# Optimization experiments

Hardware: AMD Instinct MI355X
Metric: run time of the kernel (lower is better)

Reference implementation:

```python
import jax, jax.numpy as jnp
import numpy as np

N_NODES = 50000
N_EDGES = 800000
IN_FEAT = 128
HID = 128
OUT = 10
N_GRAPHS = 128
BN_EPS = 1e-5


def setup_inputs() -> dict:
    key = jax.random.key(0)
    ks = jax.random.split(key, 16)
    inp = {
        "n_feat": jax.random.normal(ks[0], (N_NODES, IN_FEAT), dtype=jnp.float32),
        "src": jax.random.randint(ks[1], (N_EDGES,), 0, N_NODES),
        "dst": jax.random.randint(ks[2], (N_EDGES,), 0, N_NODES),
        "graph_ids": jnp.sort(jax.random.randint(ks[3], (N_NODES,), 0, N_GRAPHS)),
        # GraphConv weights (DGL layout: weight [in, out], bias [out])
        "W1": jax.random.normal(ks[4], (IN_FEAT, HID), dtype=jnp.float32) / np.sqrt(IN_FEAT),
        "b1": jnp.zeros((HID,), dtype=jnp.float32),
        "W2": jax.random.normal(ks[5], (HID, HID), dtype=jnp.float32) / np.sqrt(HID),
        "b2": jnp.zeros((HID,), dtype=jnp.float32),
        # BatchNorm1d affine params
        "gamma": jnp.ones((HID,), dtype=jnp.float32),
        "beta": jnp.zeros((HID,), dtype=jnp.float32),
        # MLP head
        "fc1_w": jax.random.normal(ks[6], (HID, HID), dtype=jnp.float32) / np.sqrt(HID),
        "fc1_b": jnp.zeros((HID,), dtype=jnp.float32),
        "fc2_w": jax.random.normal(ks[7], (HID, OUT), dtype=jnp.float32) / np.sqrt(HID),
        "fc2_b": jnp.zeros((OUT,), dtype=jnp.float32),
    }
    return inp


def _graph_conv(x, W, b, src, dst, inv_sqrt_out, inv_sqrt_in):
    # DGL GraphConv, norm='both': h = D_in^{-1/2} A D_out^{-1/2} x W + b
    h = x * inv_sqrt_out[:, None]          # [N, d_in]
    h = h @ W                              # [N, d_out] (project before gather: fewer bytes moved)
    agg = jax.ops.segment_sum(h[src], dst, num_segments=N_NODES)  # gather + scatter-add
    return agg * inv_sqrt_in[:, None] + b


def reference(n_feat, src, dst, graph_ids, W1, b1, W2, b2, gamma, beta,
              fc1_w, fc1_b, fc2_w, fc2_b):
    ones_e = jnp.ones((N_EDGES,), dtype=jnp.float32)
    deg_out = jnp.clip(jax.ops.segment_sum(ones_e, src, num_segments=N_NODES), 1.0)
    deg_in = jnp.clip(jax.ops.segment_sum(ones_e, dst, num_segments=N_NODES), 1.0)
    inv_sqrt_out = jax.lax.rsqrt(deg_out)
    inv_sqrt_in = jax.lax.rsqrt(deg_in)

    x = jax.nn.relu(_graph_conv(n_feat, W1, b1, src, dst, inv_sqrt_out, inv_sqrt_in))
    # dropout is identity in eval mode
    x = jax.nn.relu(_graph_conv(x, W2, b2, src, dst, inv_sqrt_out, inv_sqrt_in))

    # SumPooling over graphs
    embedding = jax.ops.segment_sum(x, graph_ids, num_segments=N_GRAPHS)  # [B, HID]

    # BatchNorm1d (training-mode batch stats, biased variance like torch)
    mu = jnp.mean(embedding, axis=0)
    var = jnp.mean(jnp.square(embedding - mu), axis=0)
    h = gamma * (embedding - mu) * jax.lax.rsqrt(var + BN_EPS) + beta

    h = jax.nn.relu(h @ fc1_w + fc1_b)
    logits = h @ fc2_w + fc2_b
    return embedding, jax.nn.log_softmax(logits, axis=-1)
```

## Files before the change

kernel.cpp:

```cpp
#include <hip/hip_runtime.h>
#include <hip/hip_bf16.h>
#include <math.h>

#define N_NODES 50000
#define N_EDGES 800000
#define HID 128
#define N_GRAPHS 128
#define OUTC 10
#define BN_EPS 1e-5f

#define SCAN_B 256
#define N_SCAN_BLOCKS ((N_NODES + SCAN_B - 1) / SCAN_B)

#define POOL_CHUNK 32
#define N_POOL_BLOCKS ((N_NODES + POOL_CHUNK - 1) / POOL_CHUNK)

#define HB 80
#define HWORDS (N_NODES / 2)
#define HR_B 128
#define HR_BLOCKS ((HWORDS + HR_B - 1) / HR_B)

#define EPAD 8
#define E_SRC_CAP (N_EDGES + N_NODES * EPAD)

#define LDA 136

#define MM1_ROWS 320
#define MM1_SLICES (MM1_ROWS / 16)
#define MM1_TILES ((N_NODES + 1 + MM1_ROWS - 1) / MM1_ROWS)

#define AGG_NODES 16
#define AGG_BLOCKS (N_NODES / AGG_NODES)

typedef short short8 __attribute__((ext_vector_type(8)));
typedef float floatx4 __attribute__((ext_vector_type(4)));

template <typename T, typename F>
__device__ inline T bitcast(F f) {
    union { F a; T b; } u;
    u.a = f;
    return u.b;
}

__device__ inline unsigned short f2bf(float x) {
    return __hip_bfloat16_raw(__float2bfloat16(x)).x;
}

__global__ __launch_bounds__(1024) void hist_part_kernel(const int* __restrict__ src,
                                                         const int* __restrict__ dst,
                                                         unsigned int* __restrict__ part,
                                                         const float* __restrict__ W1,
                                                         const float* __restrict__ W2,
                                                         unsigned short* __restrict__ Wp) {
    if (blockIdx.x == 2 * HB) {
        for (int q = threadIdx.x; q < 4096; q += 1024) {
            int wi = q >> 11;
            const float* __restrict__ W = wi ? W2 : W1;
            int t2 = q & 2047;
            int tile = t2 >> 6, lane = t2 & 63;
            int kc = tile >> 3, nt = tile & 7;
            int n = lane & 15, quad = lane >> 4;
            unsigned short v[8];
#pragma unroll
            for (int j = 0; j < 8; j++) {
                int k = kc * 32 + quad * 8 + j;
                v[j] = f2bf(W[k * HID + nt * 16 + n]);
            }
            *(uint4*)&Wp[(size_t)q * 8] = *(uint4*)v;
        }
        return;
    }
    __shared__ unsigned int h[HWORDS];
    for (int i = threadIdx.x; i < HWORDS; i += 1024) h[i] = 0;
    __syncthreads();
    int half = (blockIdx.x >= HB) ? 1 : 0;
    const int* __restrict__ idx = half ? dst : src;
    int b = blockIdx.x - half * HB;
    for (int e = b * 1024 + threadIdx.x; e < N_EDGES; e += HB * 1024) {
        int v = idx[e];
        atomicAdd(&h[v >> 1], 1u << ((v & 1) << 4));
    }
    __syncthreads();
    unsigned int* __restrict__ out = part + (size_t)blockIdx.x * HWORDS;
    for (int i = threadIdx.x; i < HWORDS; i += 1024) out[i] = h[i];
}

__global__ __launch_bounds__(HR_B) void hist_reduce_kernel(unsigned int* __restrict__ part,
                                                           int* __restrict__ cnt_in,
                                                           float* __restrict__ inv_out,
                                                           float* __restrict__ inv_in,
                                                           int* __restrict__ bsum) {
    int w = blockIdx.x * HR_B + threadIdx.x;
    int padsum = 0;
    if (w < HWORDS) {
        unsigned int s = 0, d = 0;
        for (int b = 0; b < HB; b++) {
            s += part[(size_t)b * HWORDS + w];
            unsigned int c = part[(size_t)(b + HB) * HWORDS + w];
            part[(size_t)(b + HB) * HWORDS + w] = d;
            d += c;
        }
        int i0 = w * 2, i1 = i0 + 1;
        int so0 = (int)(s & 0xFFFFu), so1 = (int)(s >> 16);
        int di0 = (int)(d & 0xFFFFu), di1 = (int)(d >> 16);
        cnt_in[i0] = di0;
        cnt_in[i1] = di1;
        inv_out[i0] = rsqrtf(fmaxf((float)so0, 1.0f));
        inv_out[i1] = rsqrtf(fmaxf((float)so1, 1.0f));
        inv_in[i0] = rsqrtf(fmaxf((float)di0, 1.0f));
        inv_in[i1] = rsqrtf(fmaxf((float)di1, 1.0f));
        padsum = ((di0 + EPAD - 1) & ~(EPAD - 1)) + ((di1 + EPAD - 1) & ~(EPAD - 1));
    }
    __shared__ int red[HR_B];
    red[threadIdx.x] = padsum;
    __syncthreads();
    for (int o = HR_B / 2; o > 0; o >>= 1) {
        if (threadIdx.x < o) red[threadIdx.x] += red[threadIdx.x + o];
        __syncthreads();
    }
    if (threadIdx.x == 0) bsum[blockIdx.x] = red[0];
}

__global__ void scan_write_kernel(const int* __restrict__ cnt, const int* __restrict__ bsum,
                                  int* __restrict__ row_ptr, int* __restrict__ edge_src) {
    __shared__ int sb[SCAN_B];
    __shared__ int part[SCAN_B];
    int t = threadIdx.x;
    sb[t] = (t < N_SCAN_BLOCKS) ? bsum[t] : 0;
    __syncthreads();
    for (int off = 1; off < SCAN_B; off <<= 1) {
        int u = (t >= off) ? sb[t - off] : 0;
        __syncthreads();
        sb[t] += u;
        __syncthreads();
    }
    int boff = (blockIdx.x == 0) ? 0 : sb[blockIdx.x - 1];

    int i = blockIdx.x * SCAN_B + t;
    int raw = (i < N_NODES) ? cnt[i] : 0;
    int v = (raw + EPAD - 1) & ~(EPAD - 1);
    part[t] = v;
    __syncthreads();
    for (int off = 1; off < SCAN_B; off <<= 1) {
        int u = (t >= off) ? part[t - off] : 0;
        __syncthreads();
        part[t] += u;
        __syncthreads();
    }
    if (i < N_NODES) {
        int ex = part[t] - v + boff;
        row_ptr[i] = ex;
        for (int p = ex + raw; p < ex + v; p++) edge_src[p] = N_NODES;
        if (i == N_NODES - 1) row_ptr[N_NODES] = ex + v;
    }
}

__device__ inline void mm_slice16(const unsigned short* __restrict__ xs,
                                  const unsigned short* __restrict__ Wp,
                                  __hip_bfloat16* __restrict__ Y, int row0, int rowl) {
    int lane = threadIdx.x & 63;
    int m = lane & 15, quad = lane >> 4;

    short8 a[4];
#pragma unroll
    for (int kc = 0; kc < 4; kc++)
        a[kc] = bitcast<short8>(*(const uint4*)&xs[(rowl + m) * LDA + kc * 32 + quad * 8]);

    floatx4 acc[8];
#pragma unroll
    for (int nt = 0; nt < 8; nt++) acc[nt] = (floatx4){0.f, 0.f, 0.f, 0.f};

#pragma unroll
    for (int nt = 0; nt < 8; nt++) {
#pragma unroll
        for (int kc = 0; kc < 4; kc++) {
            short8 bfr = bitcast<short8>(
                *(const uint4*)&Wp[((size_t)(kc * 8 + nt) * 64 + lane) * 8]);
            acc[nt] = __builtin_amdgcn_mfma_f32_16x16x32_bf16(a[kc], bfr, acc[nt], 0, 0, 0);
        }
    }

#pragma unroll
    for (int nt = 0; nt < 8; nt++) {
#pragma unroll
        for (int i = 0; i < 4; i++) {
            int rg = row0 + rowl + quad * 4 + i;
            if (rg < N_NODES + 1) {
                Y[(size_t)rg * HID + nt * 16 + m] = __float2bfloat16(acc[nt][i]);
            }
        }
    }
}

__global__ __launch_bounds__(1024) void csrmm1_kernel(const int* __restrict__ src,
                                                      const int* __restrict__ dst,
                                                      const unsigned int* __restrict__ part,
                                                      const int* __restrict__ row_ptr,
                                                      int* __restrict__ edge_src,
                                                      const float* __restrict__ X,
                                                      const float* __restrict__ scale,
                                                      const unsigned short* __restrict__ Wp,
                                                      __hip_bfloat16* __restrict__ Y,
                                                      float* __restrict__ emb) {
    __shared__ unsigned int shb[HWORDS];
    int t = threadIdx.x, b = blockIdx.x;

    if (b < HB) {
        unsigned int* loc = shb;
        const unsigned int* __restrict__ off = part + (size_t)(b + HB) * HWORDS;
        for (int i = t; i < HWORDS; i += 1024) loc[i] = off[i];
        __syncthreads();
        for (int e = b * 1024 + t; e < N_EDGES; e += HB * 1024) {
            int d = dst[e];
            unsigned int old = atomicAdd(&loc[d >> 1], 1u << ((d & 1) << 4));
            int local = (d & 1) ? (int)(old >> 16) : (int)(old & 0xFFFFu);
            edge_src[row_ptr[d] + local] = src[e];
        }
        return;
    }
    if (b == HB + MM1_TILES) {
        for (int i = t; i < N_GRAPHS * HID; i += 1024) emb[i] = 0.f;
        return;
    }

    unsigned short* xs = (unsigned short*)shb;
    int row0 = (b - HB) * MM1_ROWS;
    for (int j = 0; j < MM1_ROWS / 32; j++) {
        int idx4 = j * 1024 + t;
        int r = idx4 >> 5;
        int col = (idx4 & 31) * 4;
        int rg = row0 + r;
        float4 v = make_float4(0.f, 0.f, 0.f, 0.f);
        if (rg < N_NODES) {
            v = *(const float4*)&X[(size_t)rg * HID + col];
            float sc = scale[rg];
            v.x *= sc; v.y *= sc; v.z *= sc; v.w *= sc;
        }
        unsigned short o[4];
        o[0] = f2bf(v.x); o[1] = f2bf(v.y); o[2] = f2bf(v.z); o[3] = f2bf(v.w);
        *(ushort4*)&xs[r * LDA + col] = *(ushort4*)o;
    }
    __syncthreads();
    int wave = t >> 6;
    for (int sl = wave; sl < MM1_SLICES; sl += 16)
        mm_slice16(xs, Wp, Y, row0, sl * 16);
}

#define ACC8(u)                                                                              \
    acc[0] += __uint_as_float(u.x << 16); acc[1] += __uint_as_float(u.x & 0xFFFF0000u);      \
    acc[2] += __uint_as_float(u.y << 16); acc[3] += __uint_as_float(u.y & 0xFFFF0000u);      \
    acc[4] += __uint_as_float(u.z << 16); acc[5] += __uint_as_float(u.z & 0xFFFF0000u);      \
    acc[6] += __uint_as_float(u.w << 16); acc[7] += __uint_as_float(u.w & 0xFFFF0000u);

__global__ __launch_bounds__(256) void agg1mm2_kernel(const __hip_bfloat16* __restrict__ Y1,
                                                      const int* __restrict__ edge_src,
                                                      const int* __restrict__ row_ptr,
                                                      const float* __restrict__ inv_in,
                                                      const float* __restrict__ inv_out,
                                                      const float* __restrict__ bias,
                                                      const unsigned short* __restrict__ Wp2,
                                                      __hip_bfloat16* __restrict__ Y2) {
    if (blockIdx.x == AGG_BLOCKS) {
        if (threadIdx.x < 16) {
            uint4 z = make_uint4(0u, 0u, 0u, 0u);
            *(uint4*)&Y2[(size_t)N_NODES * HID + threadIdx.x * 8] = z;
        }
        return;
    }
    __shared__ unsigned short xs[AGG_NODES * LDA];
    const uint4* __restrict__ Yq = (const uint4*)Y1;
    int wave = threadIdx.x >> 6;
    int lane = threadIdx.x & 63;
    int esub = lane >> 4;
    int f16 = lane & 15;

    for (int it = 0; it < 4; it++) {
        int n = blockIdx.x * AGG_NODES + wave * 4 + it;
        int beg = row_ptr[n], end = row_ptr[n + 1];
        float acc[8] = {};
        for (int base = beg; base < end; base += 64) {
            int mm = min(64, end - base);
            int idx = (lane < mm) ? edge_src[base + lane] : N_NODES;
            int j = 0;
            for (; j + 16 <= mm; j += 16) {
                int s0 = __shfl(idx, j + esub);
                int s1 = __shfl(idx, j + 4 + esub);
                int s2 = __shfl(idx, j + 8 + esub);
                int s3 = __shfl(idx, j + 12 + esub);
                uint4 u0 = Yq[s0 * (HID / 8) + f16];
                uint4 u1 = Yq[s1 * (HID / 8) + f16];
                uint4 u2 = Yq[s2 * (HID / 8) + f16];
                uint4 u3 = Yq[s3 * (HID / 8) + f16];
                ACC8(u0); ACC8(u1); ACC8(u2); ACC8(u3);
            }
            if (j < mm) {
                int s0 = __shfl(idx, j + esub);
                int s1 = __shfl(idx, j + 4 + esub);
                uint4 u0 = Yq[s0 * (HID / 8) + f16];
                uint4 u1 = Yq[s1 * (HID / 8) + f16];
                ACC8(u0); ACC8(u1);
            }
        }
#pragma unroll
        for (int i = 0; i < 8; i++) {
            acc[i] += __shfl_xor(acc[i], 16);
            acc[i] += __shfl_xor(acc[i], 32);
        }
        if (lane < 16) {
            float si = inv_in[n];
            float so = inv_out[n];
            int f0 = f16 * 8;
            float4 b0 = *(const float4*)&bias[f0];
            float4 b1 = *(const float4*)&bias[f0 + 4];
            unsigned short u[8];
            u[0] = f2bf(fmaxf(acc[0] * si + b0.x, 0.f) * so);
            u[1] = f2bf(fmaxf(acc[1] * si + b0.y, 0.f) * so);
            u[2] = f2bf(fmaxf(acc[2] * si + b0.z, 0.f) * so);
            u[3] = f2bf(fmaxf(acc[3] * si + b0.w, 0.f) * so);
            u[4] = f2bf(fmaxf(acc[4] * si + b1.x, 0.f) * so);
            u[5] = f2bf(fmaxf(acc[5] * si + b1.y, 0.f) * so);
            u[6] = f2bf(fmaxf(acc[6] * si + b1.z, 0.f) * so);
            u[7] = f2bf(fmaxf(acc[7] * si + b1.w, 0.f) * so);
            *(uint4*)&xs[(wave * 4 + it) * LDA + f0] = *(uint4*)u;
        }
    }
    __syncthreads();

    int m = lane & 15, quad = lane >> 4;
    short8 a[4];
#pragma unroll
    for (int kc = 0; kc < 4; kc++)
        a[kc] = bitcast<short8>(*(const uint4*)&xs[m * LDA + kc * 32 + quad * 8]);
#pragma unroll
    for (int w2 = 0; w2 < 2; w2++) {
        int nt = wave * 2 + w2;
        floatx4 acc2 = (floatx4){0.f, 0.f, 0.f, 0.f};
#pragma unroll
        for (int kc = 0; kc < 4; kc++) {
            short8 bfr = bitcast<short8>(
                *(const uint4*)&Wp2[((size_t)(kc * 8 + nt) * 64 + lane) * 8]);
            acc2 = __builtin_amdgcn_mfma_f32_16x16x32_bf16(a[kc], bfr, acc2, 0, 0, 0);
        }
#pragma unroll
        for (int i = 0; i < 4; i++) {
            int rg = blockIdx.x * AGG_NODES + quad * 4 + i;
            Y2[(size_t)rg * HID + nt * 16 + m] = __float2bfloat16(acc2[i]);
        }
    }
}

__global__ __launch_bounds__(256) void agg2_kernel(const __hip_bfloat16* __restrict__ Y,
                                                   const int* __restrict__ edge_src,
                                                   const int* __restrict__ row_ptr,
                                                   const float* __restrict__ inv_in,
                                                   const float* __restrict__ bias,
                                                   float* __restrict__ Xout) {
    const uint4* __restrict__ Yq = (const uint4*)Y;
    int wave = threadIdx.x >> 6;
    int lane = threadIdx.x & 63;
    int n = blockIdx.x * 4 + wave;
    if (n >= N_NODES) return;
    int beg = row_ptr[n], end = row_ptr[n + 1];
    int esub = lane >> 4;
    int f16 = lane & 15;
    float acc[8] = {};
    for (int base = beg; base < end; base += 64) {
        int mm = min(64, end - base);
        int idx = (lane < mm) ? edge_src[base + lane] : N_NODES;
        int j = 0;
        for (; j + 16 <= mm; j += 16) {
            int s0 = __shfl(idx, j + esub);
            int s1 = __shfl(idx, j + 4 + esub);
            int s2 = __shfl(idx, j + 8 + esub);
            int s3 = __shfl(idx, j + 12 + esub);
            uint4 u0 = Yq[s0 * (HID / 8) + f16];
            uint4 u1 = Yq[s1 * (HID / 8) + f16];
            uint4 u2 = Yq[s2 * (HID / 8) + f16];
            uint4 u3 = Yq[s3 * (HID / 8) + f16];
            ACC8(u0); ACC8(u1); ACC8(u2); ACC8(u3);
        }
        if (j < mm) {
            int s0 = __shfl(idx, j + esub);
            int s1 = __shfl(idx, j + 4 + esub);
            uint4 u0 = Yq[s0 * (HID / 8) + f16];
            uint4 u1 = Yq[s1 * (HID / 8) + f16];
            ACC8(u0); ACC8(u1);
        }
    }
#pragma unroll
    for (int i = 0; i < 8; i++) {
        acc[i] += __shfl_xor(acc[i], 16);
        acc[i] += __shfl_xor(acc[i], 32);
    }
    if (lane < 16) {
        float si = inv_in[n];
        int f0 = f16 * 8;
        float4 b0 = *(const float4*)&bias[f0];
        float4 b1 = *(const float4*)&bias[f0 + 4];
        float4 o0, o1;
        o0.x = fmaxf(acc[0] * si + b0.x, 0.f);
        o0.y = fmaxf(acc[1] * si + b0.y, 0.f);
        o0.z = fmaxf(acc[2] * si + b0.z, 0.f);
        o0.w = fmaxf(acc[3] * si + b0.w, 0.f);
        o1.x = fmaxf(acc[4] * si + b1.x, 0.f);
        o1.y = fmaxf(acc[5] * si + b1.y, 0.f);
        o1.z = fmaxf(acc[6] * si + b1.z, 0.f);
        o1.w = fmaxf(acc[7] * si + b1.w, 0.f);
        *(float4*)&Xout[(size_t)n * HID + f0] = o0;
        *(float4*)&Xout[(size_t)n * HID + f0 + 4] = o1;
    }
}

__global__ __launch_bounds__(64) void pool_kernel(const float* __restrict__ X,
                                                  const int* __restrict__ gid,
                                                  float* __restrict__ emb) {
    int lane = threadIdx.x;
    int n0 = blockIdx.x * POOL_CHUNK;
    int n1 = min(n0 + POOL_CHUNK, N_NODES);
    if (n0 >= N_NODES) return;
    int g_cur = gid[n0];
    float ax = 0.f, ay = 0.f;
    for (int n = n0; n < n1; n++) {
        int g = gid[n];
        if (g != g_cur) {
            atomicAdd(&emb[g_cur * HID + lane * 2], ax);
            atomicAdd(&emb[g_cur * HID + lane * 2 + 1], ay);
            ax = 0.f; ay = 0.f;
            g_cur = g;
        }
        float2 v = *(const float2*)&X[(size_t)n * HID + lane * 2];
        ax += v.x;
        ay += v.y;
    }
    atomicAdd(&emb[g_cur * HID + lane * 2], ax);
    atomicAdd(&emb[g_cur * HID + lane * 2 + 1], ay);
}

__global__ __launch_bounds__(128) void head_fused_kernel(const float* __restrict__ emb,
                                                         const float* __restrict__ gamma,
                                                         const float* __restrict__ beta,
                                                         const float* __restrict__ fc1_w,
                                                         const float* __restrict__ fc1_b,
                                                         const float* __restrict__ fc2_w,
                                                         const float* __restrict__ fc2_b,
                                                         float* __restrict__ out) {
    int r = blockIdx.x, f = threadIdx.x;
    float s = 0.f;
    for (int row = 0; row < N_GRAPHS; row++) s += emb[row * HID + f];
    float mu = s * (1.f / N_GRAPHS);
    float v = 0.f;
    for (int row = 0; row < N_GRAPHS; row++) {
        float d = emb[row * HID + f] - mu;
        v += d * d;
    }
    v *= (1.f / N_GRAPHS);
    float sc = gamma[f] * rsqrtf(v + BN_EPS);
    float sh = beta[f] - mu * sc;

    __shared__ float xr[HID];
    xr[f] = emb[r * HID + f] * sc + sh;
    __syncthreads();
    float acc = fc1_b[f];
    for (int k = 0; k < HID; k++) acc += xr[k] * fc1_w[k * HID + f];
    __shared__ float hr[HID];
    hr[f] = fmaxf(acc, 0.f);
    __syncthreads();

    __shared__ float logits[OUTC];
    __shared__ float mstat[2];
    if (f < OUTC) {
        float a = fc2_b[f];
        for (int k = 0; k < HID; k++) a += hr[k] * fc2_w[k * OUTC + f];
        logits[f] = a;
    }
    __syncthreads();
    if (f == 0) {
        float m = logits[0];
        for (int o = 1; o < OUTC; o++) m = fmaxf(m, logits[o]);
        float sum = 0.f;
        for (int o = 0; o < OUTC; o++) sum += expf(logits[o] - m);
        mstat[0] = m;
        mstat[1] = logf(sum);
    }
    __syncthreads();
    if (f < OUTC) out[r * OUTC + f] = logits[f] - mstat[0] - mstat[1];
}

extern "C" void kernel_launch(void* const* d_in, const int* in_sizes, int n_in,
                              void* d_out, int out_size, void* d_ws, size_t ws_size,
                              hipStream_t stream) {
    const float* n_feat = (const float*)d_in[0];
    const int*   src    = (const int*)d_in[1];
    const int*   dst    = (const int*)d_in[2];
    const int*   gid    = (const int*)d_in[3];
    const float* W1     = (const float*)d_in[4];
    const float* b1     = (const float*)d_in[5];
    const float* W2     = (const float*)d_in[6];
    const float* b2     = (const float*)d_in[7];
    const float* gamma  = (const float*)d_in[8];
    const float* beta   = (const float*)d_in[9];
    const float* fc1_w  = (const float*)d_in[10];
    const float* fc1_b  = (const float*)d_in[11];
    const float* fc2_w  = (const float*)d_in[12];
    const float* fc2_b  = (const float*)d_in[13];

    char* wsb = (char*)d_ws;
    size_t off = 0;
    auto alloc = [&](size_t bytes) -> void* {
        void* p = wsb + off;
        off += (bytes + 255) & ~(size_t)255;
        return p;
    };
    int*   cnt_in  = (int*)alloc((size_t)N_NODES * 4);
    int*   row_ptr = (int*)alloc((size_t)(N_NODES + 1) * 4);
    int*   e_src   = (int*)alloc((size_t)E_SRC_CAP * 4);
    float* inv_out = (float*)alloc((size_t)N_NODES * 4);
    float* inv_in  = (float*)alloc((size_t)N_NODES * 4);
    unsigned int* part = (unsigned int*)alloc((size_t)2 * HB * HWORDS * 4);
    __hip_bfloat16* Y1 = (__hip_bfloat16*)alloc((size_t)(N_NODES + 1) * HID * 2);
    __hip_bfloat16* Y2 = (__hip_bfloat16*)alloc((size_t)(N_NODES + 1) * HID * 2);
    float* X       = (float*)alloc((size_t)N_NODES * HID * 4);
    unsigned short* Wp = (unsigned short*)alloc((size_t)2 * 32 * 64 * 8 * 2);
    int*   bsum    = (int*)alloc((size_t)SCAN_B * 4);

    float* emb_out = (float*)d_out;
    float* lsm_out = emb_out + N_GRAPHS * HID;

    hist_part_kernel<<<2 * HB + 1, 1024, 0, stream>>>(src, dst, part, W1, W2, Wp);
    hist_reduce_kernel<<<HR_BLOCKS, HR_B, 0, stream>>>(part, cnt_in, inv_out, inv_in, bsum);
    scan_write_kernel<<<N_SCAN_BLOCKS, SCAN_B, 0, stream>>>(cnt_in, bsum, row_ptr, e_src);
    csrmm1_kernel<<<HB + MM1_TILES + 1, 1024, 0, stream>>>(src, dst, part, row_ptr, e_src,
                                                           n_feat, inv_out, Wp, Y1, emb_out);
    agg1mm2_kernel<<<AGG_BLOCKS + 1, 256, 0, stream>>>(Y1, e_src, row_ptr, inv_in, inv_out,
                                                       b1, Wp + (size_t)32 * 64 * 8, Y2);
    agg2_kernel<<<(N_NODES + 3) / 4, 256, 0, stream>>>(Y2, e_src, row_ptr, inv_in, b2, X);

    pool_kernel<<<N_POOL_BLOCKS, 64, 0, stream>>>(X, gid, emb_out);
    head_fused_kernel<<<N_GRAPHS, HID, 0, stream>>>(emb_out, gamma, beta, fc1_w, fc1_b,
                                                    fc2_w, fc2_b, lsm_out);
}
```

Baseline: 257.7 us.

## Fuse degree scan with first projection GEMM and split CSR fill into own kernel

The prefix scan that builds row_ptr now runs in the same launch as the first feature projection (X*inv_out @ W1), which only depends on inv_out. The projection uses 64-row tiles with 256-thread blocks instead of 320-row tiles with 1024 threads. The CSR edge fill, which needs row_ptr, moves into its own kernel after this launch. This regrouping keeps the kernel count the same while hiding the serial scan behind GEMM work and giving the GEMM smaller blocks that need less shared memory, so occupancy can rise. The fill kernel still needs its large shared histogram and no longer overlaps with the GEMM.

```diff
diff --git a/kernel.cpp b/kernel.cpp
--- a/kernel.cpp
+++ b/kernel.cpp
@@ -25,9 +25,7 @@
 
 #define LDA 136
 
-#define MM1_ROWS 320
-#define MM1_SLICES (MM1_ROWS / 16)
-#define MM1_TILES ((N_NODES + 1 + MM1_ROWS - 1) / MM1_ROWS)
+#define MM_BLOCKS ((N_NODES + 64) / 64)
 
 #define AGG_NODES 16
 #define AGG_BLOCKS (N_NODES / AGG_NODES)
@@ -121,45 +119,13 @@
     if (threadIdx.x == 0) bsum[blockIdx.x] = red[0];
 }
 
-__global__ void scan_write_kernel(const int* __restrict__ cnt, const int* __restrict__ bsum,
-                                  int* __restrict__ row_ptr, int* __restrict__ edge_src) {
-    __shared__ int sb[SCAN_B];
-    __shared__ int part[SCAN_B];
-    int t = threadIdx.x;
-    sb[t] = (t < N_SCAN_BLOCKS) ? bsum[t] : 0;
-    __syncthreads();
-    for (int off = 1; off < SCAN_B; off <<= 1) {
-        int u = (t >= off) ? sb[t - off] : 0;
-        __syncthreads();
-        sb[t] += u;
-        __syncthreads();
-    }
-    int boff = (blockIdx.x == 0) ? 0 : sb[blockIdx.x - 1];
-
-    int i = blockIdx.x * SCAN_B + t;
-    int raw = (i < N_NODES) ? cnt[i] : 0;
-    int v = (raw + EPAD - 1) & ~(EPAD - 1);
-    part[t] = v;
-    __syncthreads();
-    for (int off = 1; off < SCAN_B; off <<= 1) {
-        int u = (t >= off) ? part[t - off] : 0;
-        __syncthreads();
-        part[t] += u;
-        __syncthreads();
-    }
-    if (i < N_NODES) {
-        int ex = part[t] - v + boff;
-        row_ptr[i] = ex;
-        for (int p = ex + raw; p < ex + v; p++) edge_src[p] = N_NODES;
-        if (i == N_NODES - 1) row_ptr[N_NODES] = ex + v;
-    }
-}
-
-__device__ inline void mm_slice16(const unsigned short* __restrict__ xs,
-                                  const unsigned short* __restrict__ Wp,
-                                  __hip_bfloat16* __restrict__ Y, int row0, int rowl) {
-    int lane = threadIdx.x & 63;
+__device__ inline void mm_tail(const unsigned short* __restrict__ xs,
+                               const unsigned short* __restrict__ Wp,
+                               __hip_bfloat16* __restrict__ Y, int row0) {
+    int tid = threadIdx.x;
+    int wave = tid >> 6, lane = tid & 63;
     int m = lane & 15, quad = lane >> 4;
+    int rowl = wave * 16;
 
     short8 a[4];
 #pragma unroll
@@ -192,58 +158,92 @@
     }
 }
 
-__global__ __launch_bounds__(1024) void csrmm1_kernel(const int* __restrict__ src,
-                                                      const int* __restrict__ dst,
-                                                      const unsigned int* __restrict__ part,
-                                                      const int* __restrict__ row_ptr,
+__global__ __launch_bounds__(256) void scanmm1_kernel(const int* __restrict__ cnt,
+                                                      const int* __restrict__ bsum,
+                                                      int* __restrict__ row_ptr,
                                                       int* __restrict__ edge_src,
                                                       const float* __restrict__ X,
                                                       const float* __restrict__ scale,
                                                       const unsigned short* __restrict__ Wp,
                                                       __hip_bfloat16* __restrict__ Y,
                                                       float* __restrict__ emb) {
-    __shared__ unsigned int shb[HWORDS];
-    int t = threadIdx.x, b = blockIdx.x;
-
-    if (b < HB) {
-        unsigned int* loc = shb;
-        const unsigned int* __restrict__ off = part + (size_t)(b + HB) * HWORDS;
-        for (int i = t; i < HWORDS; i += 1024) loc[i] = off[i];
+    __shared__ unsigned short xs[64 * LDA];
+    int t = threadIdx.x;
+    int b = blockIdx.x;
+
+    if (b >= N_SCAN_BLOCKS) {
+        if (b == N_SCAN_BLOCKS + MM_BLOCKS) {
+            for (int i = t; i < N_GRAPHS * HID; i += 256) emb[i] = 0.f;
+            return;
+        }
+        int row0 = (b - N_SCAN_BLOCKS) * 64;
+        for (int j = 0; j < 8; j++) {
+            int idx4 = j * 256 + t;
+            int r = idx4 >> 5;
+            int col = (idx4 & 31) * 4;
+            int rg = row0 + r;
+            float4 v = make_float4(0.f, 0.f, 0.f, 0.f);
+            if (rg < N_NODES) {
+                v = *(const float4*)&X[(size_t)rg * HID + col];
+                float sc = scale[rg];
+                v.x *= sc; v.y *= sc; v.z *= sc; v.w *= sc;
+            }
+            unsigned short o[4];
+            o[0] = f2bf(v.x); o[1] = f2bf(v.y); o[2] = f2bf(v.z); o[3] = f2bf(v.w);
+            *(ushort4*)&xs[r * LDA + col] = *(ushort4*)o;
+        }
         __syncthreads();
-        for (int e = b * 1024 + t; e < N_EDGES; e += HB * 1024) {
-            int d = dst[e];
-            unsigned int old = atomicAdd(&loc[d >> 1], 1u << ((d & 1) << 4));
-            int local = (d & 1) ? (int)(old >> 16) : (int)(old & 0xFFFFu);
-            edge_src[row_ptr[d] + local] = src[e];
-        }
+        mm_tail(xs, Wp, Y, row0);
         return;
     }
-    if (b == HB + MM1_TILES) {
-        for (int i = t; i < N_GRAPHS * HID; i += 1024) emb[i] = 0.f;
-        return;
-    }
-
-    unsigned short* xs = (unsigned short*)shb;
-    int row0 = (b - HB) * MM1_ROWS;
-    for (int j = 0; j < MM1_ROWS / 32; j++) {
-        int idx4 = j * 1024 + t;
-        int r = idx4 >> 5;
-        int col = (idx4 & 31) * 4;
-        int rg = row0 + r;
-        float4 v = make_float4(0.f, 0.f, 0.f, 0.f);
-        if (rg < N_NODES) {
-            v = *(const float4*)&X[(size_t)rg * HID + col];
-            float sc = scale[rg];
-            v.x *= sc; v.y *= sc; v.z *= sc; v.w *= sc;
-        }
-        unsigned short o[4];
-        o[0] = f2bf(v.x); o[1] = f2bf(v.y); o[2] = f2bf(v.z); o[3] = f2bf(v.w);
-        *(ushort4*)&xs[r * LDA + col] = *(ushort4*)o;
-    }
-    __syncthreads();
-    int wave = t >> 6;
-    for (int sl = wave; sl < MM1_SLICES; sl += 16)
-        mm_slice16(xs, Wp, Y, row0, sl * 16);
+
+    int* sb = (int*)xs;
+    int* part = (int*)xs + 256;
+    sb[t] = (t < N_SCAN_BLOCKS) ? bsum[t] : 0;
+    __syncthreads();
+    for (int off = 1; off < SCAN_B; off <<= 1) {
+        int u = (t >= off) ? sb[t - off] : 0;
+        __syncthreads();
+        sb[t] += u;
+        __syncthreads();
+    }
+    int boff = (b == 0) ? 0 : sb[b - 1];
+
+    int i = b * SCAN_B + t;
+    int raw = (i < N_NODES) ? cnt[i] : 0;
+    int v = (raw + EPAD - 1) & ~(EPAD - 1);
+    part[t] = v;
+    __syncthreads();
+    for (int off = 1; off < SCAN_B; off <<= 1) {
+        int u = (t >= off) ? part[t - off] : 0;
+        __syncthreads();
+        part[t] += u;
+        __syncthreads();
+    }
+    if (i < N_NODES) {
+        int ex = part[t] - v + boff;
+        row_ptr[i] = ex;
+        for (int p = ex + raw; p < ex + v; p++) edge_src[p] = N_NODES;
+        if (i == N_NODES - 1) row_ptr[N_NODES] = ex + v;
+    }
+}
+
+__global__ __launch_bounds__(1024) void csr_fill_kernel(const int* __restrict__ src,
+                                                        const int* __restrict__ dst,
+                                                        const unsigned int* __restrict__ part,
+                                                        const int* __restrict__ row_ptr,
+                                                        int* __restrict__ edge_src) {
+    __shared__ unsigned int loc[HWORDS];
+    int b = blockIdx.x;
+    const unsigned int* __restrict__ off = part + (size_t)(b + HB) * HWORDS;
+    for (int i = threadIdx.x; i < HWORDS; i += 1024) loc[i] = off[i];
+    __syncthreads();
+    for (int e = b * 1024 + threadIdx.x; e < N_EDGES; e += HB * 1024) {
+        int d = dst[e];
+        unsigned int old = atomicAdd(&loc[d >> 1], 1u << ((d & 1) << 4));
+        int local = (d & 1) ? (int)(old >> 16) : (int)(old & 0xFFFFu);
+        edge_src[row_ptr[d] + local] = src[e];
+    }
 }
 
 #define ACC8(u)                                                                              \
@@ -528,9 +528,10 @@
 
     hist_part_kernel<<<2 * HB + 1, 1024, 0, stream>>>(src, dst, part, W1, W2, Wp);
     hist_reduce_kernel<<<HR_BLOCKS, HR_B, 0, stream>>>(part, cnt_in, inv_out, inv_in, bsum);
-    scan_write_kernel<<<N_SCAN_BLOCKS, SCAN_B, 0, stream>>>(cnt_in, bsum, row_ptr, e_src);
-    csrmm1_kernel<<<HB + MM1_TILES + 1, 1024, 0, stream>>>(src, dst, part, row_ptr, e_src,
-                                                           n_feat, inv_out, Wp, Y1, emb_out);
+    scanmm1_kernel<<<N_SCAN_BLOCKS + MM_BLOCKS + 1, 256, 0, stream>>>(
+        cnt_in, bsum, row_ptr, e_src, n_feat, inv_out, Wp, Y1, emb_out);
+    csr_fill_kernel<<<HB, 1024, 0, stream>>>(src, dst, part, row_ptr, e_src);
+
     agg1mm2_kernel<<<AGG_BLOCKS + 1, 256, 0, stream>>>(Y1, e_src, row_ptr, inv_in, inv_out,
                                                        b1, Wp + (size_t)32 * 64 * 8, Y2);
     agg2_kernel<<<(N_NODES + 3) / 4, 256, 0, stream>>>(Y2, e_src, row_ptr, inv_in, b2, X);
```

New measurement: 242.1 us. -6.0%, faster.
